# Kernel optimization log

Measured on AMD Instinct MI355X. Metric: run time of the kernel, lower is better.

## Reference

```python
import jax, jax.numpy as jnp
import numpy as np

B, T, C, H = 2, 2048, 1024, 16
HD = C // H  # head_dim = 64

def _rope(x, cos, sin):
    # x: [B,H,T,HD]; cos/sin: [T,HD//2]
    x2 = x.reshape(*x.shape[:-1], HD // 2, 2)
    x0, x1 = x2[..., 0], x2[..., 1]
    # complex multiply (x0 + i x1) * (cos + i sin)
    o0 = x0 * cos - x1 * sin
    o1 = x0 * sin + x1 * cos
    return jnp.stack([o0, o1], axis=-1).reshape(x.shape)

def setup_inputs() -> dict:
    key = jax.random.key(0)
    k1, k2, k3 = jax.random.split(key, 3)
    x = jax.random.normal(k1, (B, T, C), dtype=jnp.float32)
    w_qkv = jax.random.normal(k2, (C, 3 * C), dtype=jnp.float32) * (1.0 / np.sqrt(C))
    w_proj = jax.random.normal(k3, (C, C), dtype=jnp.float32) * (1.0 / np.sqrt(C))
    # standard RoPE frequencies: theta_j = 10000^(-2j/HD), angles t*theta_j
    inv_freq = 1.0 / (10000.0 ** (np.arange(0, HD, 2, dtype=np.float32) / HD))  # [HD//2]
    ang = np.arange(T, dtype=np.float32)[:, None] * inv_freq[None, :]           # [T,HD//2]
    return {"x": x, "w_qkv": w_qkv, "w_proj": w_proj,
            "freqs_cos": jnp.asarray(np.cos(ang)), "freqs_sin": jnp.asarray(np.sin(ang))}

def reference(x, w_qkv, w_proj, freqs_cos, freqs_sin):
    qkv = x @ w_qkv                                   # [B,T,3C]
    q, k, v = jnp.split(qkv, 3, axis=-1)
    def heads(t):
        return t.reshape(B, T, H, HD).transpose(0, 2, 1, 3)  # [B,H,T,HD]
    q, k, v = heads(q), heads(k), heads(v)
    q = _rope(q, freqs_cos, freqs_sin)
    k = _rope(k, freqs_cos, freqs_sin)
    scores = jnp.einsum('bhqd,bhkd->bhqk', q, k) * (1.0 / np.sqrt(HD))
    causal = jnp.tril(jnp.ones((T, T), dtype=bool))
    scores = jnp.where(causal, scores, jnp.finfo(scores.dtype).min)
    attn = jax.nn.softmax(scores, axis=-1)
    y = jnp.einsum('bhqk,bhkd->bhqd', attn, v)        # [B,H,T,HD]
    y = y.transpose(0, 2, 1, 3).reshape(B, T, C)
    return y @ w_proj
```

## Files before the change

### kernel.cpp

```cpp
#include <hip/hip_runtime.h>

typedef float  floatx4 __attribute__((ext_vector_type(4)));
typedef _Float16 half8 __attribute__((ext_vector_type(8)));
typedef _Float16 half4v __attribute__((ext_vector_type(4)));

__device__ __forceinline__ void gld16(const void* g, void* l) {
    __builtin_amdgcn_global_load_lds(
        (const __attribute__((address_space(1))) void*)g,
        (__attribute__((address_space(3))) void*)l, 16, 0, 0);
}

__global__ __launch_bounds__(256) void conv_x_kernel(const float* __restrict__ x,
                                                     _Float16* __restrict__ xh) {
    int i = blockIdx.x * 256 + threadIdx.x;
    float4 v = ((const float4*)x)[i];
    half4v o = { (_Float16)v.x, (_Float16)v.y, (_Float16)v.z, (_Float16)v.w };
    ((half4v*)xh)[i] = o;
}

__global__ __launch_bounds__(256) void transpose_f32f16(const float* __restrict__ W,
                                                        _Float16* __restrict__ WT,
                                                        int K, int N) {
    __shared__ _Float16 t[64][72];
    int n0 = blockIdx.x * 64, k0 = blockIdx.y * 64;
    int c = threadIdx.x & 63, r4 = threadIdx.x >> 6;
    for (int rr = 0; rr < 64; rr += 4) {
        int k = k0 + rr + r4;
        t[rr + r4][c] = (_Float16)W[(size_t)k * N + n0 + c];
    }
    __syncthreads();
    for (int rr = 0; rr < 64; rr += 4) {
        int n = n0 + rr + r4;
        WT[(size_t)n * K + k0 + c] = t[c][rr + r4];
    }
}

__global__ __launch_bounds__(256) void gemm_tn(const _Float16* __restrict__ A,
                                               const _Float16* __restrict__ BT,
                                               _Float16* __restrict__ Cf16,
                                               int M, int N, int K) {
    __shared__ __align__(16) _Float16 sAB[2 * 128 * 32];
    _Float16* sA = sAB;
    _Float16* sB = sAB + 128 * 32;

    const int tid  = threadIdx.x;
    const int wave = tid >> 6, lane = tid & 63;
    const int lrow = lane & 15, quad = lane >> 4;
    const int bm = blockIdx.x * 128, bn = blockIdx.y * 128;
    const int waveM = (wave >> 1) * 64, waveN = (wave & 1) * 64;

    floatx4 acc[4][4] = {};

    const int r0 = tid >> 2,          k80 = (tid & 3) * 8;
    const int r1 = (tid + 256) >> 2,  k81 = ((tid + 256) & 3) * 8;
    _Float16* lA0 = sA + (wave * 64) * 8;
    _Float16* lA1 = sA + (wave * 64 + 256) * 8;
    _Float16* lB0 = sB + (wave * 64) * 8;
    _Float16* lB1 = sB + (wave * 64 + 256) * 8;
    const _Float16* A0 = A + (size_t)(bm + r0) * K + k80;
    const _Float16* A1 = A + (size_t)(bm + r1) * K + k81;
    const _Float16* B0 = BT + (size_t)(bn + r0) * K + k80;
    const _Float16* B1 = BT + (size_t)(bn + r1) * K + k81;

    for (int k0 = 0; k0 < K; k0 += 32) {
        gld16(A0 + k0, lA0);
        gld16(A1 + k0, lA1);
        gld16(B0 + k0, lB0);
        gld16(B1 + k0, lB1);
        __syncthreads();

        half8 aF[4], bF[4];
#pragma unroll
        for (int mt = 0; mt < 4; ++mt)
            aF[mt] = *(const half8*)&sA[(waveM + mt * 16 + lrow) * 32 + quad * 8];
#pragma unroll
        for (int nt = 0; nt < 4; ++nt)
            bF[nt] = *(const half8*)&sB[(waveN + nt * 16 + lrow) * 32 + quad * 8];
#pragma unroll
        for (int mt = 0; mt < 4; ++mt)
#pragma unroll
            for (int nt = 0; nt < 4; ++nt)
                acc[mt][nt] = __builtin_amdgcn_mfma_f32_16x16x32_f16(
                    aF[mt], bF[nt], acc[mt][nt], 0, 0, 0);
        __syncthreads();
    }

    _Float16* ep = sAB + wave * 1152;
    const int erow = lane >> 3, ecol = (lane & 7) * 8;
#pragma unroll
    for (int mt = 0; mt < 4; ++mt) {
#pragma unroll
        for (int nt = 0; nt < 4; ++nt)
#pragma unroll
            for (int r = 0; r < 4; ++r)
                ep[(quad * 4 + r) * 72 + nt * 16 + lrow] = (_Float16)acc[mt][nt][r];
        __builtin_amdgcn_wave_barrier();
#pragma unroll
        for (int st = 0; st < 2; ++st) {
            uint4 d = *(const uint4*)&ep[(st * 8 + erow) * 72 + ecol];
            *(uint4*)&Cf16[(size_t)(bm + waveM + mt * 16 + st * 8 + erow) * N +
                           bn + waveN + ecol] = d;
        }
        __builtin_amdgcn_wave_barrier();
    }
}

__global__ __launch_bounds__(256) void gemm_tn64(const _Float16* __restrict__ A,
                                                 const _Float16* __restrict__ BT,
                                                 float* __restrict__ C,
                                                 int M, int N, int K) {
    __shared__ __align__(16) _Float16 sA[64 * 32];
    __shared__ __align__(16) _Float16 sB[128 * 32];

    const int tid  = threadIdx.x;
    const int wave = tid >> 6, lane = tid & 63;
    const int lrow = lane & 15, quad = lane >> 4;
    const int bm = blockIdx.x * 64, bn = blockIdx.y * 128;
    const int waveM = (wave >> 1) * 32, waveN = (wave & 1) * 64;

    floatx4 acc[2][4] = {};

    const int ra = tid >> 2, k8 = (tid & 3) * 8;
    const int rb1 = (tid + 256) >> 2, k8b = ((tid + 256) & 3) * 8;
    const _Float16* Ap  = A + (size_t)(bm + ra) * K + k8;
    const _Float16* Bp0 = BT + (size_t)(bn + ra) * K + k8;
    const _Float16* Bp1 = BT + (size_t)(bn + rb1) * K + k8b;
    _Float16* lA  = sA + tid * 8;
    _Float16* lB0 = sB + (wave * 64) * 8;
    _Float16* lB1 = sB + (wave * 64 + 256) * 8;

    for (int k0 = 0; k0 < K; k0 += 32) {
        gld16(Ap + k0, lA);
        gld16(Bp0 + k0, lB0);
        gld16(Bp1 + k0, lB1);
        __syncthreads();

        half8 aF[2], bF[4];
#pragma unroll
        for (int mt = 0; mt < 2; ++mt)
            aF[mt] = *(const half8*)&sA[(waveM + mt * 16 + lrow) * 32 + quad * 8];
#pragma unroll
        for (int nt = 0; nt < 4; ++nt)
            bF[nt] = *(const half8*)&sB[(waveN + nt * 16 + lrow) * 32 + quad * 8];
#pragma unroll
        for (int mt = 0; mt < 2; ++mt)
#pragma unroll
            for (int nt = 0; nt < 4; ++nt)
                acc[mt][nt] = __builtin_amdgcn_mfma_f32_16x16x32_f16(
                    aF[mt], bF[nt], acc[mt][nt], 0, 0, 0);
        __syncthreads();
    }

#pragma unroll
    for (int mt = 0; mt < 2; ++mt)
#pragma unroll
        for (int nt = 0; nt < 4; ++nt)
#pragma unroll
            for (int r = 0; r < 4; ++r) {
                int row = bm + waveM + mt * 16 + quad * 4 + r;
                int col = bn + waveN + nt * 16 + lrow;
                C[(size_t)row * N + col] = acc[mt][nt][r];
            }
}

__global__ __launch_bounds__(256) void rope_vt(const _Float16* __restrict__ qkv,
                                               const float* __restrict__ fc,
                                               const float* __restrict__ fs,
                                               _Float16* __restrict__ qh,
                                               _Float16* __restrict__ kh,
                                               _Float16* __restrict__ vt) {
    __shared__ _Float16 s[64][72];
    const int bh = blockIdx.y, b = bh >> 4, h = bh & 15;
    const int t0 = blockIdx.x * 64;
    const int tid = threadIdx.x;

    {
        int c4 = (tid & 15) * 4;
        int j0 = c4 >> 1;
        int rr = tid >> 4;
#pragma unroll
        for (int pass = 0; pass < 4; ++pass) {
            int tt = t0 + pass * 16 + rr;
            const _Float16* src = qkv + (size_t)(b * 2048 + tt) * 3072 + h * 64 + c4;
            float c0 = fc[tt * 32 + j0],     s0 = fs[tt * 32 + j0];
            float c1 = fc[tt * 32 + j0 + 1], s1 = fs[tt * 32 + j0 + 1];
            half4v qv = *(const half4v*)(src);
            half4v kv = *(const half4v*)(src + 1024);
            half4v qo, ko;
            {
                float x0 = (float)qv[0], x1 = (float)qv[1];
                qo[0] = (_Float16)(x0 * c0 - x1 * s0); qo[1] = (_Float16)(x0 * s0 + x1 * c0);
                x0 = (float)qv[2]; x1 = (float)qv[3];
                qo[2] = (_Float16)(x0 * c1 - x1 * s1); qo[3] = (_Float16)(x0 * s1 + x1 * c1);
                x0 = (float)kv[0]; x1 = (float)kv[1];
                ko[0] = (_Float16)(x0 * c0 - x1 * s0); ko[1] = (_Float16)(x0 * s0 + x1 * c0);
                x0 = (float)kv[2]; x1 = (float)kv[3];
                ko[2] = (_Float16)(x0 * c1 - x1 * s1); ko[3] = (_Float16)(x0 * s1 + x1 * c1);
            }
            size_t o = ((size_t)bh * 2048 + tt) * 64 + c4;
            *(half4v*)&qh[o] = qo;
            *(half4v*)&kh[o] = ko;
        }
    }
    {
        int c = tid & 63, r4 = tid >> 6;
        const _Float16* srcv = qkv + 2048 + h * 64;
        for (int rr = 0; rr < 64; rr += 4)
            s[rr + r4][c] = srcv[(size_t)(b * 2048 + t0 + rr + r4) * 3072 + c];
        __syncthreads();
        for (int rr = 0; rr < 64; rr += 4)
            vt[((size_t)bh * 64 + rr + r4) * 2048 + t0 + c] = s[c][rr + r4];
    }
}

#define U_(qc,k0,k1,dir,slot) ((qc)|((k0)<<5)|((k1)<<11)|((dir)<<17)|((slot)<<18))
__device__ const unsigned int UTAB[24] = {
    U_(15, 0,15,0,14), U_(15,16,31,0,15), U_( 7, 0,15,1, 0),
    U_(14, 0,14,0,12), U_(14,15,29,0,13),
    U_(13, 0,13,0,10), U_(13,14,27,0,11), U_( 6, 0,13,1, 0),
    U_(12, 0,12,0, 8), U_(12,13,25,0, 9),
    U_(11, 0,11,0, 6), U_(11,12,23,0, 7), U_( 5, 0,11,1, 0),
    U_(10, 0,10,0, 4), U_(10,11,21,0, 5),
    U_( 9, 0, 9,0, 2), U_( 9,10,19,0, 3), U_( 4, 0, 9,1, 0),
    U_( 8, 0, 8,0, 0), U_( 8, 9,17,0, 1),
    U_( 3, 0, 7,1, 0), U_( 2, 0, 5,1, 0), U_( 1, 0, 3,1, 0), U_( 0, 0, 1,1, 0)
};

__global__ __launch_bounds__(256, 3) void attn_sk2(const _Float16* __restrict__ Q,
                                                   const _Float16* __restrict__ Kk,
                                                   const _Float16* __restrict__ Vt,
                                                   _Float16* __restrict__ Y,
                                                   _Float16* __restrict__ Opart,
                                                   float* __restrict__ lpart) {
    __shared__ __align__(16) _Float16 sK[64 * 64];
    __shared__ __align__(16) _Float16 sV[64 * 64];
    __shared__ __align__(16) _Float16 sP[128 * 72];

    const int bh = blockIdx.x, b = bh >> 4, h = bh & 15;
    const unsigned e = UTAB[blockIdx.y];
    const int qc = e & 31, k0 = (e >> 5) & 63, k1 = (e >> 11) & 63;
    const int dir = (e >> 17) & 1, slot = (e >> 18) & 15;
    const int d0 = 2 * qc, d1 = 2 * qc + 1;

    const int tid = threadIdx.x;
    const int wave = tid >> 6, lane = tid & 63;
    const int lq = lane & 15, quad = lane >> 4;

    const _Float16* Kbase = Kk + (size_t)bh * 2048 * 64;
    const _Float16* Vbase = Vt + (size_t)bh * 64 * 2048;

    const _Float16 qscale = (_Float16)(0.125f * 1.44269504f);
    half8 qF[2][2];
#pragma unroll
    for (int g = 0; g < 2; ++g) {
        const _Float16* Qp = Q + ((size_t)bh * 2048 + qc * 128 + g * 64 + wave * 16 + lq) * 64;
#pragma unroll
        for (int ks = 0; ks < 2; ++ks)
            qF[g][ks] = (*(const half8*)(Qp + ks * 32 + quad * 8)) * qscale;
    }

    floatx4 O0[4] = {}, O1[4] = {};
    float lacc0 = 0.f, lacc1 = 0.f;

    for (int kt = k0; kt <= k1; ++kt) {
        const bool live0 = (kt <= d0);
        const _Float16* kb = Kbase + (size_t)kt * 64 * 64;
        const _Float16* vb = Vbase + kt * 64;
#pragma unroll
        for (int hlf = 0; hlf < 2; ++hlf) {
            int s = tid + hlf * 256;
            int row = s >> 3;
            int ccg = (s & 7) ^ (row & 7);
            gld16(kb + row * 64 + ccg * 8, sK + s * 8);
            gld16(vb + (size_t)row * 2048 + ccg * 8, sV + s * 8);
        }
        __syncthreads();

        half4v P0[4], P1[4];
#pragma unroll
        for (int kt4 = 0; kt4 < 4; ++kt4) {
            half8 kf0 = *(const half8*)&sK[(kt4 * 16 + lq) * 64 + ((quad ^ (lq & 7)) * 8)];
            half8 kf1 = *(const half8*)&sK[(kt4 * 16 + lq) * 64 + (((4 + quad) ^ (lq & 7)) * 8)];
            floatx4 s1 = { -12.f, -12.f, -12.f, -12.f };
            s1 = __builtin_amdgcn_mfma_f32_16x16x32_f16(kf0, qF[1][0], s1, 0, 0, 0);
            s1 = __builtin_amdgcn_mfma_f32_16x16x32_f16(kf1, qF[1][1], s1, 0, 0, 0);
            if (kt == d1) {
#pragma unroll
                for (int r = 0; r < 4; ++r)
                    if (kt4 * 16 + quad * 4 + r > wave * 16 + lq) s1[r] = -1e30f;
            }
#pragma unroll
            for (int r = 0; r < 4; ++r) s1[r] = __builtin_amdgcn_exp2f(s1[r]);
            lacc1 += s1[0] + s1[1] + s1[2] + s1[3];
            P1[kt4] = half4v{ (_Float16)s1[0], (_Float16)s1[1],
                              (_Float16)s1[2], (_Float16)s1[3] };
            if (live0) {
                floatx4 s0 = { -12.f, -12.f, -12.f, -12.f };
                s0 = __builtin_amdgcn_mfma_f32_16x16x32_f16(kf0, qF[0][0], s0, 0, 0, 0);
                s0 = __builtin_amdgcn_mfma_f32_16x16x32_f16(kf1, qF[0][1], s0, 0, 0, 0);
                if (kt == d0) {
#pragma unroll
                    for (int r = 0; r < 4; ++r)
                        if (kt4 * 16 + quad * 4 + r > wave * 16 + lq) s0[r] = -1e30f;
                }
#pragma unroll
                for (int r = 0; r < 4; ++r) s0[r] = __builtin_amdgcn_exp2f(s0[r]);
                lacc0 += s0[0] + s0[1] + s0[2] + s0[3];
                P0[kt4] = half4v{ (_Float16)s0[0], (_Float16)s0[1],
                                  (_Float16)s0[2], (_Float16)s0[3] };
            }
        }

        _Float16* pw1 = &sP[(64 + wave * 16 + lq) * 72];
#pragma unroll
        for (int kt4 = 0; kt4 < 4; ++kt4)
            *(half4v*)(pw1 + kt4 * 16 + quad * 4) = P1[kt4];
        _Float16* pw0 = &sP[(wave * 16 + lq) * 72];
        if (live0) {
#pragma unroll
            for (int kt4 = 0; kt4 < 4; ++kt4)
                *(half4v*)(pw0 + kt4 * 16 + quad * 4) = P0[kt4];
        }
        __builtin_amdgcn_wave_barrier();

        half8 aP0[2], aP1[2];
#pragma unroll
        for (int ks = 0; ks < 2; ++ks) {
            aP1[ks] = *(const half8*)(pw1 + ks * 32 + quad * 8);
            if (live0) aP0[ks] = *(const half8*)(pw0 + ks * 32 + quad * 8);
        }
#pragma unroll
        for (int nt = 0; nt < 4; ++nt)
#pragma unroll
            for (int ks = 0; ks < 2; ++ks) {
                half8 vf = *(const half8*)&sV[(nt * 16 + lq) * 64 +
                                              (((ks * 4 + quad) ^ (lq & 7)) * 8)];
                O1[nt] = __builtin_amdgcn_mfma_f32_16x16x32_f16(aP1[ks], vf, O1[nt], 0, 0, 0);
                if (live0)
                    O0[nt] = __builtin_amdgcn_mfma_f32_16x16x32_f16(aP0[ks], vf, O0[nt], 0, 0, 0);
            }
        __syncthreads();
    }

#pragma unroll
    for (int g = 0; g < 2; ++g) {
        float l = g ? lacc1 : lacc0;
        l += __shfl_xor(l, 16);
        l += __shfl_xor(l, 32);
        floatx4* O = g ? O1 : O0;
        if (dir) {
            float invl = 1.0f / l;
#pragma unroll
            for (int r = 0; r < 4; ++r) {
                float iv = __shfl(invl, (lane & 48) | (quad * 4 + r));
                int q = qc * 128 + g * 64 + wave * 16 + quad * 4 + r;
                size_t rowoff = ((size_t)b * 2048 + q) * 1024 + h * 64;
#pragma unroll
                for (int nt = 0; nt < 4; ++nt)
                    Y[rowoff + nt * 16 + lq] = (_Float16)(O[nt][r] * iv);
            }
        } else {
            int gslot = bh * 16 + slot;
            _Float16* op = Opart + (size_t)gslot * 8192;
#pragma unroll
            for (int r = 0; r < 4; ++r) {
                int row = g * 64 + wave * 16 + quad * 4 + r;
#pragma unroll
                for (int nt = 0; nt < 4; ++nt)
                    op[row * 64 + nt * 16 + lq] = (_Float16)O[nt][r];
            }
            if (quad == 0)
                lpart[gslot * 128 + g * 64 + wave * 16 + lq] = l;
        }
    }
}

__global__ __launch_bounds__(256) void attn_reduce2(const _Float16* __restrict__ Opart,
                                                    const float* __restrict__ lpart,
                                                    _Float16* __restrict__ Y) {
    const int bh = blockIdx.x, b = bh >> 4, h = bh & 15;
    const int qcx = blockIdx.y, qc = 8 + qcx;
    const int g0 = bh * 16 + qcx * 2, g1 = g0 + 1;
    const int tid = threadIdx.x;

#pragma unroll
    for (int it = 0; it < 2; ++it) {
        int idx = tid + it * 256;
        int row = idx >> 2, cs = (idx & 3) * 16;
        const _Float16* p0 = Opart + (size_t)g0 * 8192 + row * 64 + cs;
        const _Float16* p1 = Opart + (size_t)g1 * 8192 + row * 64 + cs;
        float invl = 1.0f / (lpart[g0 * 128 + row] + lpart[g1 * 128 + row]);
        half8 a0 = *(const half8*)p0, a1 = *(const half8*)(p0 + 8);
        half8 b0 = *(const half8*)p1, b1 = *(const half8*)(p1 + 8);
        half8 o0, o1;
#pragma unroll
        for (int i = 0; i < 8; ++i) {
            o0[i] = (_Float16)(((float)a0[i] + (float)b0[i]) * invl);
            o1[i] = (_Float16)(((float)a1[i] + (float)b1[i]) * invl);
        }
        _Float16* y = Y + ((size_t)b * 2048 + qc * 128 + row) * 1024 + h * 64 + cs;
        *(half8*)y = o0;
        *(half8*)(y + 8) = o1;
    }
}

extern "C" void kernel_launch(void* const* d_in, const int* in_sizes, int n_in,
                              void* d_out, int out_size, void* d_ws, size_t ws_size,
                              hipStream_t stream) {
    const float* x     = (const float*)d_in[0];
    const float* wqkv  = (const float*)d_in[1];
    const float* wproj = (const float*)d_in[2];
    const float* fc    = (const float*)d_in[3];
    const float* fs    = (const float*)d_in[4];
    float* out = (float*)d_out;

    char* ws = (char*)d_ws;
    _Float16* xh    = (_Float16*)(ws);
    _Float16* wqT   = (_Float16*)(ws + ((size_t)8  << 20));
    _Float16* wpT   = (_Float16*)(ws + ((size_t)14 << 20));
    _Float16* qkvh  = (_Float16*)(ws + ((size_t)16 << 20));
    _Float16* qh    = (_Float16*)(ws + ((size_t)40 << 20));
    _Float16* kh    = (_Float16*)(ws + ((size_t)48 << 20));
    _Float16* vt    = (_Float16*)(ws + ((size_t)56 << 20));
    _Float16* yh    = xh;
    _Float16* Opart = qkvh;
    float*    lpartf= (float*)(ws + ((size_t)26 << 20));

    conv_x_kernel<<<4096, 256, 0, stream>>>(x, xh);
    transpose_f32f16<<<dim3(48, 16), 256, 0, stream>>>(wqkv, wqT, 1024, 3072);
    transpose_f32f16<<<dim3(16, 16), 256, 0, stream>>>(wproj, wpT, 1024, 1024);
    gemm_tn<<<dim3(32, 24), 256, 0, stream>>>(xh, wqT, qkvh, 4096, 3072, 1024);
    rope_vt<<<dim3(32, 32), 256, 0, stream>>>(qkvh, fc, fs, qh, kh, vt);
    attn_sk2<<<dim3(32, 24), 256, 0, stream>>>(qh, kh, vt, yh, Opart, lpartf);
    attn_reduce2<<<dim3(32, 8), 256, 0, stream>>>(Opart, lpartf, yh);
    gemm_tn64<<<dim3(64, 8), 256, 0, stream>>>(yh, wpT, out, 4096, 1024, 1024);
}
```

Measured before the change: 190.5 us.

## Swizzle GEMM LDS layouts and deepen K tile to 64 in QKV GEMM

The 128x128 GEMM now loads a K-tile of 64 per iteration, halving the barrier count, and XOR-swizzles the 16-byte chunk index by row so fragment reads from LDS avoid bank conflicts. The 64x128 output GEMM gets the same XOR swizzle on its 32-wide K tiles. LDS use for the big GEMM doubles to 32KB, which could lower occupancy. Loads are still not double-buffered.

```diff
diff --git a/kernel.cpp b/kernel.cpp
--- a/kernel.cpp
+++ b/kernel.cpp
@@ -39,9 +39,9 @@
                                                const _Float16* __restrict__ BT,
                                                _Float16* __restrict__ Cf16,
                                                int M, int N, int K) {
-    __shared__ __align__(16) _Float16 sAB[2 * 128 * 32];
+    __shared__ __align__(16) _Float16 sAB[2 * 128 * 64];
     _Float16* sA = sAB;
-    _Float16* sB = sAB + 128 * 32;
+    _Float16* sB = sAB + 128 * 64;
 
     const int tid  = threadIdx.x;
     const int wave = tid >> 6, lane = tid & 63;
@@ -51,37 +51,41 @@
 
     floatx4 acc[4][4] = {};
 
-    const int r0 = tid >> 2,          k80 = (tid & 3) * 8;
-    const int r1 = (tid + 256) >> 2,  k81 = ((tid + 256) & 3) * 8;
-    _Float16* lA0 = sA + (wave * 64) * 8;
-    _Float16* lA1 = sA + (wave * 64 + 256) * 8;
-    _Float16* lB0 = sB + (wave * 64) * 8;
-    _Float16* lB1 = sB + (wave * 64 + 256) * 8;
-    const _Float16* A0 = A + (size_t)(bm + r0) * K + k80;
-    const _Float16* A1 = A + (size_t)(bm + r1) * K + k81;
-    const _Float16* B0 = BT + (size_t)(bn + r0) * K + k80;
-    const _Float16* B1 = BT + (size_t)(bn + r1) * K + k81;
-
-    for (int k0 = 0; k0 < K; k0 += 32) {
-        gld16(A0 + k0, lA0);
-        gld16(A1 + k0, lA1);
-        gld16(B0 + k0, lB0);
-        gld16(B1 + k0, lB1);
-        __syncthreads();
-
-        half8 aF[4], bF[4];
-#pragma unroll
-        for (int mt = 0; mt < 4; ++mt)
-            aF[mt] = *(const half8*)&sA[(waveM + mt * 16 + lrow) * 32 + quad * 8];
-#pragma unroll
-        for (int nt = 0; nt < 4; ++nt)
-            bF[nt] = *(const half8*)&sB[(waveN + nt * 16 + lrow) * 32 + quad * 8];
-#pragma unroll
-        for (int mt = 0; mt < 4; ++mt)
+    int srow[4], sccg[4];
+#pragma unroll
+    for (int hlf = 0; hlf < 4; ++hlf) {
+        int s = tid + hlf * 256;
+        srow[hlf] = s >> 3;
+        sccg[hlf] = ((s & 7) ^ (srow[hlf] & 7)) * 8;
+    }
+
+    for (int k0 = 0; k0 < K; k0 += 64) {
+#pragma unroll
+        for (int hlf = 0; hlf < 4; ++hlf) {
+            int s = tid + hlf * 256;
+            gld16(A + (size_t)(bm + srow[hlf]) * K + k0 + sccg[hlf], sA + s * 8);
+            gld16(BT + (size_t)(bn + srow[hlf]) * K + k0 + sccg[hlf], sB + s * 8);
+        }
+        __syncthreads();
+
+#pragma unroll
+        for (int kk = 0; kk < 2; ++kk) {
+            half8 aF[4], bF[4];
+#pragma unroll
+            for (int mt = 0; mt < 4; ++mt)
+                aF[mt] = *(const half8*)&sA[(waveM + mt * 16 + lrow) * 64 +
+                                            (((kk * 4 + quad) ^ (lrow & 7)) * 8)];
 #pragma unroll
             for (int nt = 0; nt < 4; ++nt)
-                acc[mt][nt] = __builtin_amdgcn_mfma_f32_16x16x32_f16(
-                    aF[mt], bF[nt], acc[mt][nt], 0, 0, 0);
+                bF[nt] = *(const half8*)&sB[(waveN + nt * 16 + lrow) * 64 +
+                                            (((kk * 4 + quad) ^ (lrow & 7)) * 8)];
+#pragma unroll
+            for (int mt = 0; mt < 4; ++mt)
+#pragma unroll
+                for (int nt = 0; nt < 4; ++nt)
+                    acc[mt][nt] = __builtin_amdgcn_mfma_f32_16x16x32_f16(
+                        aF[mt], bF[nt], acc[mt][nt], 0, 0, 0);
+        }
         __syncthreads();
     }
 
@@ -120,28 +124,33 @@
 
     floatx4 acc[2][4] = {};
 
-    const int ra = tid >> 2, k8 = (tid & 3) * 8;
-    const int rb1 = (tid + 256) >> 2, k8b = ((tid + 256) & 3) * 8;
-    const _Float16* Ap  = A + (size_t)(bm + ra) * K + k8;
-    const _Float16* Bp0 = BT + (size_t)(bn + ra) * K + k8;
-    const _Float16* Bp1 = BT + (size_t)(bn + rb1) * K + k8b;
-    _Float16* lA  = sA + tid * 8;
-    _Float16* lB0 = sB + (wave * 64) * 8;
-    _Float16* lB1 = sB + (wave * 64 + 256) * 8;
+    const int raA = tid >> 2, ccA = (((tid & 3) ^ ((tid >> 2) & 3))) * 8;
+    int rB[2], cB[2];
+#pragma unroll
+    for (int hlf = 0; hlf < 2; ++hlf) {
+        int s = tid + hlf * 256;
+        rB[hlf] = s >> 2;
+        cB[hlf] = ((s & 3) ^ ((s >> 2) & 3)) * 8;
+    }
 
     for (int k0 = 0; k0 < K; k0 += 32) {
-        gld16(Ap + k0, lA);
-        gld16(Bp0 + k0, lB0);
-        gld16(Bp1 + k0, lB1);
+        gld16(A + (size_t)(bm + raA) * K + k0 + ccA, sA + tid * 8);
+#pragma unroll
+        for (int hlf = 0; hlf < 2; ++hlf) {
+            int s = tid + hlf * 256;
+            gld16(BT + (size_t)(bn + rB[hlf]) * K + k0 + cB[hlf], sB + s * 8);
+        }
         __syncthreads();
 
         half8 aF[2], bF[4];
 #pragma unroll
         for (int mt = 0; mt < 2; ++mt)
-            aF[mt] = *(const half8*)&sA[(waveM + mt * 16 + lrow) * 32 + quad * 8];
+            aF[mt] = *(const half8*)&sA[(waveM + mt * 16 + lrow) * 32 +
+                                        ((quad ^ (lrow & 3)) * 8)];
 #pragma unroll
         for (int nt = 0; nt < 4; ++nt)
-            bF[nt] = *(const half8*)&sB[(waveN + nt * 16 + lrow) * 32 + quad * 8];
+            bF[nt] = *(const half8*)&sB[(waveN + nt * 16 + lrow) * 32 +
+                                        ((quad ^ (lrow & 3)) * 8)];
 #pragma unroll
         for (int mt = 0; mt < 2; ++mt)
 #pragma unroll
```

Measured after the change: 186.9 us. About the same (-1.9%).
